# Kernel optimization log

Hardware: AMD Instinct MI355X
Metric: run time of the kernel (lower is better)

Reference implementation:

```python
import jax, jax.numpy as jnp
import numpy as np

B, S, D, H = 2, 2048, 1024, 16
DK = D // H
NEG = -1e9


def setup_inputs() -> dict:
    key = jax.random.key(0)
    ks = jax.random.split(key, 12)
    scale = 1.0 / np.sqrt(D)
    inp = {
        'Q': jax.random.normal(ks[0], (B, S, D), jnp.float32),
        'K': jax.random.normal(ks[1], (B, S, D), jnp.float32),
        'V': jax.random.normal(ks[2], (B, S, D), jnp.float32),
        'mask': jnp.tril(jnp.ones((S, S), jnp.int32))[None, None],  # (1,1,S,S) causal
        # torch nn.Linear layout: W has shape (out, in), y = x @ W.T + b
        'WQ': jax.random.normal(ks[3], (D, D), jnp.float32) * scale,
        'bQ': jnp.zeros((D,), jnp.float32),
        'WK': jax.random.normal(ks[4], (D, D), jnp.float32) * scale,
        'bK': jnp.zeros((D,), jnp.float32),
        'WV': jax.random.normal(ks[5], (D, D), jnp.float32) * scale,
        'bV': jnp.zeros((D,), jnp.float32),
        'WO': jax.random.normal(ks[6], (D, D), jnp.float32) * scale,
        'bO': jnp.zeros((D,), jnp.float32),
    }
    return inp


def reference(Q, K, V, mask, WQ, bQ, WK, bK, WV, bV, WO, bO):
    # projections (torch Linear: x @ W.T + b), then split heads -> (B,H,S,DK)
    def split_heads(x):
        return x.reshape(B, S, H, DK).transpose(0, 2, 1, 3)

    Qh = split_heads(Q @ WQ.T + bQ)
    Kh = split_heads(K @ WK.T + bK)
    Vh = split_heads(V @ WV.T + bV)

    scores = jnp.einsum('bhqd,bhkd->bhqk', Qh, Kh) / jnp.sqrt(jnp.float32(DK))
    scores = jnp.where(mask == 0, NEG, scores)
    attn = jax.nn.softmax(scores, axis=-1)  # (B,H,S,S)
    ctx = jnp.einsum('bhqk,bhkd->bhqd', attn, Vh)
    concat = ctx.transpose(0, 2, 1, 3).reshape(B, S, D)
    out = concat @ WO.T + bO
    return out, attn
```

## Files before the change

kernel.cpp:

```cpp
#include <hip/hip_runtime.h>
#include <hip/hip_bf16.h>
#include <cstdint>
#include <cstddef>

#define S_ 2048
#define D_ 1024
#define H_ 16
#define DK_ 64
#define B_ 2

typedef unsigned short u16;
typedef __attribute__((ext_vector_type(8))) short bf16x8;
typedef __attribute__((ext_vector_type(4))) float f32x4;

__device__ inline u16 f2bf(float f) {
    union { float f; unsigned u; } c; c.f = f;
    unsigned u = c.u;
    unsigned r = (u + 0x7fffu + ((u >> 16) & 1u)) >> 16;
    return (u16)r;
}

__device__ inline uint4 cvt8(const float* __restrict__ src) {
    float4 f0 = *(const float4*)(src);
    float4 f1 = *(const float4*)(src + 4);
    union { u16 h[8]; uint4 v; } u;
    u.h[0] = f2bf(f0.x); u.h[1] = f2bf(f0.y); u.h[2] = f2bf(f0.z); u.h[3] = f2bf(f0.w);
    u.h[4] = f2bf(f1.x); u.h[5] = f2bf(f1.y); u.h[6] = f2bf(f1.z); u.h[7] = f2bf(f1.w);
    return u.v;
}

__global__ void __launch_bounds__(256)
proj_qkv(const float* __restrict__ Qi, const float* __restrict__ Ki,
         const float* __restrict__ Vi,
         const float* __restrict__ WQ, const float* __restrict__ WK,
         const float* __restrict__ WV,
         const float* __restrict__ bQ, const float* __restrict__ bK,
         const float* __restrict__ bV,
         u16* __restrict__ Qo, u16* __restrict__ Ko, u16* __restrict__ Vo)
{
    constexpr int BK  = 32;
    constexpr int BKP = 40;

    __shared__ __align__(16) u16 As[128 * BKP];
    __shared__ __align__(16) u16 Bs[128 * BKP];

    const int tid  = threadIdx.x;
    const int lane = tid & 63;
    const int wave = tid >> 6;
    const int wm = wave >> 1;
    const int wn = wave & 1;
    const int m0 = blockIdx.y * 128;
    const int n0 = blockIdx.x * 128;
    const int z  = blockIdx.z;

    const float* A    = (z == 0) ? Qi : (z == 1) ? Ki : Vi;
    const float* W    = (z == 0) ? WQ : (z == 1) ? WK : WV;
    const float* bias = (z == 0) ? bQ : (z == 1) ? bK : bV;
    u16*         O    = (z == 0) ? Qo : (z == 1) ? Ko : Vo;

    f32x4 acc[4][4];
#pragma unroll
    for (int i = 0; i < 4; ++i)
#pragma unroll
        for (int j = 0; j < 4; ++j)
            acc[i][j] = (f32x4){0.f, 0.f, 0.f, 0.f};

    const int fr = lane & 15;
    const int fk = (lane >> 4) << 3;

    for (int k0 = 0; k0 < D_; k0 += BK) {
#pragma unroll
        for (int i = 0; i < 2; ++i) {
            int linear = i * 256 + tid;
            int row = linear >> 2;
            int kk  = (linear & 3) << 3;
            *(uint4*)&As[row * BKP + kk] = cvt8(&A[(size_t)(m0 + row) * D_ + k0 + kk]);
            *(uint4*)&Bs[row * BKP + kk] = cvt8(&W[(size_t)(n0 + row) * D_ + k0 + kk]);
        }
        __syncthreads();

        bf16x8 af[4], bfv[4];
#pragma unroll
        for (int mt = 0; mt < 4; ++mt)
            af[mt] = *(const bf16x8*)&As[(wm * 64 + mt * 16 + fr) * BKP + fk];
#pragma unroll
        for (int nt = 0; nt < 4; ++nt)
            bfv[nt] = *(const bf16x8*)&Bs[(wn * 64 + nt * 16 + fr) * BKP + fk];
#pragma unroll
        for (int mt = 0; mt < 4; ++mt)
#pragma unroll
            for (int nt = 0; nt < 4; ++nt)
                acc[mt][nt] = __builtin_amdgcn_mfma_f32_16x16x32_bf16(
                    af[mt], bfv[nt], acc[mt][nt], 0, 0, 0);
        __syncthreads();
    }

#pragma unroll
    for (int mt = 0; mt < 4; ++mt)
#pragma unroll
        for (int nt = 0; nt < 4; ++nt)
#pragma unroll
            for (int r = 0; r < 4; ++r) {
                int row = m0 + wm * 64 + mt * 16 + ((lane >> 4) << 2) + r;
                int col = n0 + wn * 64 + nt * 16 + (lane & 15);
                float v = acc[mt][nt][r] + bias[col];
                size_t addr;
                if (z < 2)
                    addr = ((size_t)(row >> 11) << 21) + ((size_t)(col >> 6) << 17)
                         + ((size_t)(row & 2047) << 6) + (size_t)(col & 63);
                else
                    addr = ((size_t)(row >> 11) << 21) + ((size_t)(col >> 6) << 17)
                         + ((size_t)(col & 63) << 11) + (size_t)(row & 2047);
                O[addr] = f2bf(v);
            }
}

template<bool BF32>
__global__ void __launch_bounds__(256)
gemm_bt(const u16* __restrict__ Ab, const void* __restrict__ Bv,
        const float* __restrict__ bias, float* __restrict__ C,
        int M, int N, int K, int lda, int ldb)
{
    constexpr int BK  = 32;
    constexpr int BKP = 40;

    __shared__ __align__(16) u16 As[128 * BKP];
    __shared__ __align__(16) u16 Bs[128 * BKP];

    const int tid  = threadIdx.x;
    const int lane = tid & 63;
    const int wave = tid >> 6;
    const int wm = wave >> 1;
    const int wn = wave & 1;
    const int m0 = blockIdx.y * 128;
    const int n0 = blockIdx.x * 128;

    const float* Bf = (const float*)Bv;
    const u16*   Bb = (const u16*)Bv;

    f32x4 acc[4][4];
#pragma unroll
    for (int i = 0; i < 4; ++i)
#pragma unroll
        for (int j = 0; j < 4; ++j)
            acc[i][j] = (f32x4){0.f, 0.f, 0.f, 0.f};

    const int fr = lane & 15;
    const int fk = (lane >> 4) << 3;

    for (int k0 = 0; k0 < K; k0 += BK) {
#pragma unroll
        for (int i = 0; i < 2; ++i) {
            int linear = i * 256 + tid;
            int row = linear >> 2;
            int kk  = (linear & 3) << 3;
            *(uint4*)&As[row * BKP + kk] =
                *(const uint4*)&Ab[(size_t)(m0 + row) * lda + k0 + kk];
            *(uint4*)&Bs[row * BKP + kk] =
                BF32 ? cvt8(&Bf[(size_t)(n0 + row) * ldb + k0 + kk])
                     : *(const uint4*)&Bb[(size_t)(n0 + row) * ldb + k0 + kk];
        }
        __syncthreads();

        bf16x8 af[4], bfv[4];
#pragma unroll
        for (int mt = 0; mt < 4; ++mt)
            af[mt] = *(const bf16x8*)&As[(wm * 64 + mt * 16 + fr) * BKP + fk];
#pragma unroll
        for (int nt = 0; nt < 4; ++nt)
            bfv[nt] = *(const bf16x8*)&Bs[(wn * 64 + nt * 16 + fr) * BKP + fk];
#pragma unroll
        for (int mt = 0; mt < 4; ++mt)
#pragma unroll
            for (int nt = 0; nt < 4; ++nt)
                acc[mt][nt] = __builtin_amdgcn_mfma_f32_16x16x32_bf16(
                    af[mt], bfv[nt], acc[mt][nt], 0, 0, 0);
        __syncthreads();
    }

#pragma unroll
    for (int mt = 0; mt < 4; ++mt)
#pragma unroll
        for (int nt = 0; nt < 4; ++nt)
#pragma unroll
            for (int r = 0; r < 4; ++r) {
                int row = m0 + wm * 64 + mt * 16 + ((lane >> 4) << 2) + r;
                int col = n0 + wn * 64 + nt * 16 + (lane & 15);
                C[(size_t)row * N + col] = acc[mt][nt][r] + bias[col];
            }
}

__global__ void __launch_bounds__(256, 2)
attn_all(const u16* __restrict__ Qh, const u16* __restrict__ Kh,
         const u16* __restrict__ Vt,
         float* __restrict__ attn, u16* __restrict__ Cc)
{
    __shared__ __align__(16) u16 Qs[128 * 64];
    __shared__ __align__(16) u16 Ks[128 * 64];
    __shared__ __align__(16) u16 Vs[64 * 128];
    __shared__ __align__(16) u16 Ps[128 * 128];
    float* rowsum = (float*)Ps;

    const int tid  = threadIdx.x;
    const int lane = tid & 63;
    const int wave = tid >> 6;
    const int wm = wave >> 1, wn = wave & 1;
    const int bx = blockIdx.x;
    const int qt = (bx & 1) ? (15 - (bx >> 1)) : (bx >> 1);
    const int bh = blockIdx.y;
    const int fr = lane & 15;
    const int fq = lane >> 4;

    const u16* Qbase = Qh + (size_t)bh * S_ * DK_ + (size_t)qt * 128 * DK_;
    const u16* Kbase = Kh + (size_t)bh * S_ * DK_;
    const u16* Vbase = Vt + (size_t)bh * (size_t)DK_ * S_;
    float* out = attn + (size_t)bh * S_ * S_;

#pragma unroll
    for (int i = 0; i < 4; ++i) {
        int linear = i * 256 + tid;
        int row = linear >> 3;
        *(uint4*)((char*)Qs + (row << 7) + ((((linear & 7) << 4)) ^ ((row & 7) << 4)))
            = *(const uint4*)&Qbase[(size_t)linear << 3];
    }
    if (tid < 128) rowsum[tid] = 0.f;

    float rs[4][4];
#pragma unroll
    for (int i = 0; i < 4; ++i)
#pragma unroll
        for (int j = 0; j < 4; ++j) rs[i][j] = 0.f;

    for (int kt = 0; kt <= qt; ++kt) {
        __syncthreads();
#pragma unroll
        for (int i = 0; i < 4; ++i) {
            int linear = i * 256 + tid;
            int row = linear >> 3;
            *(uint4*)((char*)Ks + (row << 7) + ((((linear & 7) << 4)) ^ ((row & 7) << 4)))
                = *(const uint4*)&Kbase[(size_t)kt * 128 * DK_ + ((size_t)linear << 3)];
        }
        __syncthreads();

        f32x4 acc[4][4];
#pragma unroll
        for (int i = 0; i < 4; ++i)
#pragma unroll
            for (int j = 0; j < 4; ++j) acc[i][j] = (f32x4){0.f, 0.f, 0.f, 0.f};

#pragma unroll
        for (int ks = 0; ks < 64; ks += 32) {
            bf16x8 af[4], bfv[4];
#pragma unroll
            for (int mt = 0; mt < 4; ++mt) {
                int row = wm * 64 + mt * 16 + fr;
                af[mt] = *(const bf16x8*)((const char*)Qs + (row << 7)
                          + ((((ks + (fq << 3)) << 1)) ^ ((row & 7) << 4)));
            }
#pragma unroll
            for (int nt = 0; nt < 4; ++nt) {
                int row = wn * 64 + nt * 16 + fr;
                bfv[nt] = *(const bf16x8*)((const char*)Ks + (row << 7)
                          + ((((ks + (fq << 3)) << 1)) ^ ((row & 7) << 4)));
            }
#pragma unroll
            for (int mt = 0; mt < 4; ++mt)
#pragma unroll
                for (int nt = 0; nt < 4; ++nt)
                    acc[mt][nt] = __builtin_amdgcn_mfma_f32_16x16x32_bf16(
                        af[mt], bfv[nt], acc[mt][nt], 0, 0, 0);
        }

        const bool diag = (kt == qt);
#pragma unroll
        for (int mt = 0; mt < 4; ++mt)
#pragma unroll
            for (int nt = 0; nt < 4; ++nt)
#pragma unroll
                for (int r = 0; r < 4; ++r) {
                    int row = wm * 64 + mt * 16 + (fq << 2) + r;
                    int col = wn * 64 + nt * 16 + fr;
                    if (!diag || col <= row)
                        rs[mt][r] += __expf(acc[mt][nt][r] * 0.125f);
                }
    }

#pragma unroll
    for (int mt = 0; mt < 4; ++mt)
#pragma unroll
        for (int r = 0; r < 4; ++r) {
            float v = rs[mt][r];
            v += __shfl_xor(v, 1, 64);
            v += __shfl_xor(v, 2, 64);
            v += __shfl_xor(v, 4, 64);
            v += __shfl_xor(v, 8, 64);
            rs[mt][r] = v;
        }
    __syncthreads();
    if (fr == 0) {
#pragma unroll
        for (int mt = 0; mt < 4; ++mt)
#pragma unroll
            for (int r = 0; r < 4; ++r)
                atomicAdd(&rowsum[wm * 64 + mt * 16 + (fq << 2) + r], rs[mt][r]);
    }
    __syncthreads();

    float rcp[4][4];
#pragma unroll
    for (int mt = 0; mt < 4; ++mt)
#pragma unroll
        for (int r = 0; r < 4; ++r)
            rcp[mt][r] = 1.0f / rowsum[wm * 64 + mt * 16 + (fq << 2) + r];

    f32x4 cacc[4][2];
#pragma unroll
    for (int i = 0; i < 4; ++i)
#pragma unroll
        for (int j = 0; j < 2; ++j) cacc[i][j] = (f32x4){0.f, 0.f, 0.f, 0.f};

    for (int kt = 0; kt <= qt; ++kt) {
        __syncthreads();
#pragma unroll
        for (int i = 0; i < 4; ++i) {
            int linear = i * 256 + tid;
            int row = linear >> 3;
            *(uint4*)((char*)Ks + (row << 7) + ((((linear & 7) << 4)) ^ ((row & 7) << 4)))
                = *(const uint4*)&Kbase[(size_t)kt * 128 * DK_ + ((size_t)linear << 3)];
        }
#pragma unroll
        for (int i = 0; i < 4; ++i) {
            int linear = i * 256 + tid;
            int row = linear >> 4;
            int cb  = (linear & 15) << 4;
            *(uint4*)((char*)Vs + (row << 8) + (cb ^ ((row & 7) << 4)))
                = *(const uint4*)&Vbase[(size_t)row * S_ + kt * 128 + ((linear & 15) << 3)];
        }
        __syncthreads();

        f32x4 acc[4][4];
#pragma unroll
        for (int i = 0; i < 4; ++i)
#pragma unroll
            for (int j = 0; j < 4; ++j) acc[i][j] = (f32x4){0.f, 0.f, 0.f, 0.f};

#pragma unroll
        for (int ks = 0; ks < 64; ks += 32) {
            bf16x8 af[4], bfv[4];
#pragma unroll
            for (int mt = 0; mt < 4; ++mt) {
                int row = wm * 64 + mt * 16 + fr;
                af[mt] = *(const bf16x8*)((const char*)Qs + (row << 7)
                          + ((((ks + (fq << 3)) << 1)) ^ ((row & 7) << 4)));
            }
#pragma unroll
            for (int nt = 0; nt < 4; ++nt) {
                int row = wn * 64 + nt * 16 + fr;
                bfv[nt] = *(const bf16x8*)((const char*)Ks + (row << 7)
                          + ((((ks + (fq << 3)) << 1)) ^ ((row & 7) << 4)));
            }
#pragma unroll
            for (int mt = 0; mt < 4; ++mt)
#pragma unroll
                for (int nt = 0; nt < 4; ++nt)
                    acc[mt][nt] = __builtin_amdgcn_mfma_f32_16x16x32_bf16(
                        af[mt], bfv[nt], acc[mt][nt], 0, 0, 0);
        }

        const bool diag = (kt == qt);
#pragma unroll
        for (int mt = 0; mt < 4; ++mt)
#pragma unroll
            for (int nt = 0; nt < 4; ++nt)
#pragma unroll
                for (int r = 0; r < 4; ++r) {
                    int row = wm * 64 + mt * 16 + (fq << 2) + r;
                    int col = wn * 64 + nt * 16 + fr;
                    float p = 0.f;
                    if (!diag || col <= row)
                        p = __expf(acc[mt][nt][r] * 0.125f) * rcp[mt][r];
                    out[(size_t)(qt * 128 + row) * S_ + kt * 128 + col] = p;
                    *(u16*)((char*)Ps + (row << 8) + (((col << 1)) ^ ((row & 7) << 4)))
                        = f2bf(p);
                }
        __syncthreads();

#pragma unroll
        for (int ks4 = 0; ks4 < 4; ++ks4) {
            bf16x8 pf[4], vf[2];
            int kb = (ks4 * 32 + (fq << 3)) << 1;
#pragma unroll
            for (int mt = 0; mt < 4; ++mt) {
                int row = wm * 64 + mt * 16 + fr;
                pf[mt] = *(const bf16x8*)((const char*)Ps + (row << 8)
                          + (kb ^ ((row & 7) << 4)));
            }
#pragma unroll
            for (int nt = 0; nt < 2; ++nt) {
                int row = wn * 32 + nt * 16 + fr;
                vf[nt] = *(const bf16x8*)((const char*)Vs + (row << 8)
                          + (kb ^ ((row & 7) << 4)));
            }
#pragma unroll
            for (int mt = 0; mt < 4; ++mt)
#pragma unroll
                for (int nt = 0; nt < 2; ++nt)
                    cacc[mt][nt] = __builtin_amdgcn_mfma_f32_16x16x32_bf16(
                        pf[mt], vf[nt], cacc[mt][nt], 0, 0, 0);
        }
    }

#pragma unroll
    for (int mt = 0; mt < 4; ++mt)
#pragma unroll
        for (int nt = 0; nt < 2; ++nt)
#pragma unroll
            for (int r = 0; r < 4; ++r) {
                int row = wm * 64 + mt * 16 + (fq << 2) + r;
                int col = wn * 32 + nt * 16 + fr;
                size_t addr = (size_t)(bh >> 4) * S_ * D_ + (size_t)(bh & 15) * DK_
                            + (size_t)(qt * 128 + row) * D_ + col;
                Cc[addr] = f2bf(cacc[mt][nt][r]);
            }

    float4 z4 = {0.f, 0.f, 0.f, 0.f};
    for (int kt2 = qt + 1; kt2 < S_ / 128; ++kt2) {
#pragma unroll
        for (int i = 0; i < 16; ++i) {
            int linear = i * 256 + tid;
            int row = linear >> 5;
            int c   = (linear & 31) << 2;
            *(float4*)&out[(size_t)(qt * 128 + row) * S_ + kt2 * 128 + c] = z4;
        }
    }
}

extern "C" void kernel_launch(void* const* d_in, const int* in_sizes, int n_in,
                              void* d_out, int out_size, void* d_ws, size_t ws_size,
                              hipStream_t stream)
{
    const float* Q  = (const float*)d_in[0];
    const float* K  = (const float*)d_in[1];
    const float* V  = (const float*)d_in[2];
    const float* WQ = (const float*)d_in[4];
    const float* bQ = (const float*)d_in[5];
    const float* WK = (const float*)d_in[6];
    const float* bK = (const float*)d_in[7];
    const float* WV = (const float*)d_in[8];
    const float* bV = (const float*)d_in[9];
    const float* WO = (const float*)d_in[10];
    const float* bO = (const float*)d_in[11];

    float* outF  = (float*)d_out;
    float* attnF = outF + (size_t)B_ * S_ * D_;

    u16* Qh = (u16*)d_ws;
    u16* Kh = Qh + (size_t)B_ * S_ * D_;
    u16* Vt = Kh + (size_t)B_ * S_ * D_;
    u16* Cc = Vt + (size_t)B_ * S_ * D_;

    dim3 blk(256, 1, 1);
    const int M = B_ * S_;

    proj_qkv<<<dim3(D_ / 128, M / 128, 3), blk, 0, stream>>>(
        Q, K, V, WQ, WK, WV, bQ, bK, bV, Qh, Kh, Vt);

    attn_all<<<dim3(S_ / 128, B_ * H_, 1), blk, 0, stream>>>(
        Qh, Kh, Vt, attnF, Cc);

    gemm_bt<true><<<dim3(D_ / 128, M / 128, 1), blk, 0, stream>>>(
        Cc, WO, bO, outF, M, D_, D_, D_, D_);
}
```

Measured before the change: 806.9 us.

## Pre-convert inputs to bf16, use direct global-to-LDS loads and vectorized attention stores

Adds a separate kernel that converts Q, K, V and all weights to bf16 once, so the projection and output GEMMs load bf16 through global_load_lds with swizzled LDS tiles and BK=64. The attention kernel swaps the MFMA operand order so each lane owns contiguous key columns, which lets the attention-probability writes be float4 and the P tile be packed with v_cvt_pk_bf16_f32. The GEMM epilogues now also store vectorized. The aim is to cut conversion work inside the GEMM inner loops and reduce scattered scalar stores of the large attention matrix, at the cost of an extra kernel launch and more workspace traffic.

```diff
diff --git a/kernel.cpp b/kernel.cpp
--- a/kernel.cpp
+++ b/kernel.cpp
@@ -29,165 +29,209 @@
     return u.v;
 }
 
+__device__ inline unsigned pkbf(float a, float b) {
+    unsigned r;
+    asm("v_cvt_pk_bf16_f32 %0, %1, %2" : "=v"(r) : "v"(a), "v"(b));
+    return r;
+}
+
+typedef __attribute__((address_space(3))) void lds_void;
+typedef __attribute__((address_space(1))) const void glob_void;
+__device__ __forceinline__ void glds16(const u16* g, u16* l, int lane) {
+#if __has_builtin(__builtin_amdgcn_global_load_lds)
+    (void)lane;
+    __builtin_amdgcn_global_load_lds((glob_void*)g, (lds_void*)l, 16, 0, 0);
+#else
+    ((uint4*)l)[lane] = *(const uint4*)g;
+#endif
+}
+
+__device__ __forceinline__ bf16x8 rd64(const u16* arr, int row, int k) {
+    return *(const bf16x8*)((const char*)arr + (row << 7)
+             + ((k << 1) ^ ((row & 7) << 4)));
+}
+__device__ __forceinline__ bf16x8 rd128(const u16* arr, int row, int k) {
+    return *(const bf16x8*)((const char*)arr + (row << 8)
+             + ((k << 1) ^ ((row & 7) << 4)));
+}
+
 __global__ void __launch_bounds__(256)
-proj_qkv(const float* __restrict__ Qi, const float* __restrict__ Ki,
-         const float* __restrict__ Vi,
-         const float* __restrict__ WQ, const float* __restrict__ WK,
-         const float* __restrict__ WV,
+cvt_all(const float* __restrict__ Q, const float* __restrict__ K,
+        const float* __restrict__ V,
+        const float* __restrict__ WQ, const float* __restrict__ WK,
+        const float* __restrict__ WV, const float* __restrict__ WO,
+        u16* __restrict__ Qb, u16* __restrict__ Kb, u16* __restrict__ Vb,
+        u16* __restrict__ Wb)
+{
+    const size_t QN = 524288;
+    const size_t WN = 131072;
+    size_t u = (size_t)blockIdx.x * 256 + threadIdx.x;
+    const size_t total = 3 * QN + 4 * WN;
+    const size_t stride = (size_t)gridDim.x * 256;
+    for (; u < total; u += stride) {
+        const float* s; u16* d; size_t off;
+        if (u < 3 * QN) {
+            size_t seg = u / QN;
+            off = (u - seg * QN) << 3;
+            s = (seg == 0) ? Q : (seg == 1) ? K : V;
+            d = (seg == 0) ? Qb : (seg == 1) ? Kb : Vb;
+        } else {
+            size_t w = u - 3 * QN;
+            size_t seg = w / WN;
+            off = (w - seg * WN) << 3;
+            s = (seg == 0) ? WQ : (seg == 1) ? WK : (seg == 2) ? WV : WO;
+            d = Wb + seg * 1048576;
+        }
+        *(uint4*)&d[off] = cvt8(s + off);
+    }
+}
+
+__device__ __forceinline__ void gemm_core(
+    const u16* __restrict__ A, const u16* __restrict__ Bm,
+    int m0, int n0, int tid, u16* As, u16* Bs, f32x4 (&acc)[4][4])
+{
+    const int lane = tid & 63;
+    const int wave = tid >> 6;
+    const int wm = wave >> 1, wn = wave & 1;
+    const int fr = lane & 15, fq = lane >> 4;
+
+    for (int k0 = 0; k0 < 1024; k0 += 64) {
+        __syncthreads();
+#pragma unroll
+        for (int it = 0; it < 4; ++it) {
+            int linear = it * 256 + tid;
+            int row = linear >> 3, c = linear & 7;
+            glds16(&A[(size_t)(m0 + row) * 1024 + k0 + ((c ^ (row & 7)) << 3)],
+                   &As[(size_t)(it * 256 + (tid & ~63)) << 3], lane);
+        }
+#pragma unroll
+        for (int it = 0; it < 4; ++it) {
+            int linear = it * 256 + tid;
+            int row = linear >> 3, c = linear & 7;
+            glds16(&Bm[(size_t)(n0 + row) * 1024 + k0 + ((c ^ (row & 7)) << 3)],
+                   &Bs[(size_t)(it * 256 + (tid & ~63)) << 3], lane);
+        }
+        __syncthreads();
+#pragma unroll
+        for (int ks = 0; ks < 64; ks += 32) {
+            bf16x8 af[4], bfv[4];
+#pragma unroll
+            for (int mt = 0; mt < 4; ++mt)
+                af[mt] = rd64(As, wm * 64 + mt * 16 + fr, ks + (fq << 3));
+#pragma unroll
+            for (int nt = 0; nt < 4; ++nt)
+                bfv[nt] = rd64(Bs, wn * 64 + nt * 16 + fr, ks + (fq << 3));
+#pragma unroll
+            for (int mt = 0; mt < 4; ++mt)
+#pragma unroll
+                for (int nt = 0; nt < 4; ++nt)
+                    acc[mt][nt] = __builtin_amdgcn_mfma_f32_16x16x32_bf16(
+                        bfv[nt], af[mt], acc[mt][nt], 0, 0, 0);
+        }
+    }
+}
+
+__global__ void __launch_bounds__(256)
+proj_qkv(const u16* __restrict__ Qb, const u16* __restrict__ Kb,
+         const u16* __restrict__ Vb, const u16* __restrict__ Wb,
          const float* __restrict__ bQ, const float* __restrict__ bK,
          const float* __restrict__ bV,
-         u16* __restrict__ Qo, u16* __restrict__ Ko, u16* __restrict__ Vo)
+         u16* __restrict__ Qh, u16* __restrict__ Kh, u16* __restrict__ Vt)
 {
-    constexpr int BK  = 32;
-    constexpr int BKP = 40;
-
-    __shared__ __align__(16) u16 As[128 * BKP];
-    __shared__ __align__(16) u16 Bs[128 * BKP];
+    __shared__ __align__(16) u16 As[128 * 64];
+    __shared__ __align__(16) u16 Bs[128 * 64];
 
     const int tid  = threadIdx.x;
     const int lane = tid & 63;
     const int wave = tid >> 6;
-    const int wm = wave >> 1;
-    const int wn = wave & 1;
+    const int wm = wave >> 1, wn = wave & 1;
+    const int fr = lane & 15, fq = lane >> 4;
     const int m0 = blockIdx.y * 128;
     const int n0 = blockIdx.x * 128;
     const int z  = blockIdx.z;
 
-    const float* A    = (z == 0) ? Qi : (z == 1) ? Ki : Vi;
-    const float* W    = (z == 0) ? WQ : (z == 1) ? WK : WV;
+    const u16* A = (z == 0) ? Qb : (z == 1) ? Kb : Vb;
+    const u16* W = Wb + (size_t)z * 1048576;
     const float* bias = (z == 0) ? bQ : (z == 1) ? bK : bV;
-    u16*         O    = (z == 0) ? Qo : (z == 1) ? Ko : Vo;
+    u16* O = (z == 0) ? Qh : (z == 1) ? Kh : Vt;
 
     f32x4 acc[4][4];
 #pragma unroll
     for (int i = 0; i < 4; ++i)
 #pragma unroll
-        for (int j = 0; j < 4; ++j)
-            acc[i][j] = (f32x4){0.f, 0.f, 0.f, 0.f};
-
-    const int fr = lane & 15;
-    const int fk = (lane >> 4) << 3;
-
-    for (int k0 = 0; k0 < D_; k0 += BK) {
-#pragma unroll
-        for (int i = 0; i < 2; ++i) {
-            int linear = i * 256 + tid;
-            int row = linear >> 2;
-            int kk  = (linear & 3) << 3;
-            *(uint4*)&As[row * BKP + kk] = cvt8(&A[(size_t)(m0 + row) * D_ + k0 + kk]);
-            *(uint4*)&Bs[row * BKP + kk] = cvt8(&W[(size_t)(n0 + row) * D_ + k0 + kk]);
-        }
-        __syncthreads();
-
-        bf16x8 af[4], bfv[4];
-#pragma unroll
-        for (int mt = 0; mt < 4; ++mt)
-            af[mt] = *(const bf16x8*)&As[(wm * 64 + mt * 16 + fr) * BKP + fk];
-#pragma unroll
-        for (int nt = 0; nt < 4; ++nt)
-            bfv[nt] = *(const bf16x8*)&Bs[(wn * 64 + nt * 16 + fr) * BKP + fk];
-#pragma unroll
-        for (int mt = 0; mt < 4; ++mt)
-#pragma unroll
-            for (int nt = 0; nt < 4; ++nt)
-                acc[mt][nt] = __builtin_amdgcn_mfma_f32_16x16x32_bf16(
-                    af[mt], bfv[nt], acc[mt][nt], 0, 0, 0);
-        __syncthreads();
-    }
-
-#pragma unroll
-    for (int mt = 0; mt < 4; ++mt)
-#pragma unroll
-        for (int nt = 0; nt < 4; ++nt)
-#pragma unroll
-            for (int r = 0; r < 4; ++r) {
-                int row = m0 + wm * 64 + mt * 16 + ((lane >> 4) << 2) + r;
-                int col = n0 + wn * 64 + nt * 16 + (lane & 15);
-                float v = acc[mt][nt][r] + bias[col];
-                size_t addr;
-                if (z < 2)
-                    addr = ((size_t)(row >> 11) << 21) + ((size_t)(col >> 6) << 17)
-                         + ((size_t)(row & 2047) << 6) + (size_t)(col & 63);
-                else
-                    addr = ((size_t)(row >> 11) << 21) + ((size_t)(col >> 6) << 17)
-                         + ((size_t)(col & 63) << 11) + (size_t)(row & 2047);
-                O[addr] = f2bf(v);
+        for (int j = 0; j < 4; ++j) acc[i][j] = (f32x4){0.f, 0.f, 0.f, 0.f};
+
+    gemm_core(A, W, m0, n0, tid, As, Bs, acc);
+
+#pragma unroll
+    for (int mt = 0; mt < 4; ++mt) {
+#pragma unroll
+        for (int nt = 0; nt < 4; ++nt) {
+            int row  = m0 + wm * 64 + mt * 16 + fr;
+            int colb = n0 + wn * 64 + nt * 16 + (fq << 2);
+            float4 b4 = *(const float4*)&bias[colb];
+            u16 h[4];
+            h[0] = f2bf(acc[mt][nt][0] + b4.x);
+            h[1] = f2bf(acc[mt][nt][1] + b4.y);
+            h[2] = f2bf(acc[mt][nt][2] + b4.z);
+            h[3] = f2bf(acc[mt][nt][3] + b4.w);
+            if (z < 2) {
+                size_t addr = ((size_t)(row >> 11) << 21) + ((size_t)(colb >> 6) << 17)
+                            + ((size_t)(row & 2047) << 6) + (size_t)(colb & 63);
+                uint2 p; p.x = (unsigned)h[0] | ((unsigned)h[1] << 16);
+                         p.y = (unsigned)h[2] | ((unsigned)h[3] << 16);
+                *(uint2*)&O[addr] = p;
+            } else {
+#pragma unroll
+                for (int r = 0; r < 4; ++r) {
+                    int col = colb + r;
+                    size_t addr = ((size_t)(row >> 11) << 21) + ((size_t)(col >> 6) << 17)
+                                + ((size_t)(col & 63) << 11) + (size_t)(row & 2047);
+                    O[addr] = h[r];
+                }
             }
-}
-
-template<bool BF32>
+        }
+    }
+}
+
 __global__ void __launch_bounds__(256)
-gemm_bt(const u16* __restrict__ Ab, const void* __restrict__ Bv,
-        const float* __restrict__ bias, float* __restrict__ C,
-        int M, int N, int K, int lda, int ldb)
+out_gemm(const u16* __restrict__ Cc, const u16* __restrict__ WOb,
+         const float* __restrict__ bO, float* __restrict__ C)
 {
-    constexpr int BK  = 32;
-    constexpr int BKP = 40;
-
-    __shared__ __align__(16) u16 As[128 * BKP];
-    __shared__ __align__(16) u16 Bs[128 * BKP];
+    __shared__ __align__(16) u16 As[128 * 64];
+    __shared__ __align__(16) u16 Bs[128 * 64];
 
     const int tid  = threadIdx.x;
     const int lane = tid & 63;
     const int wave = tid >> 6;
-    const int wm = wave >> 1;
-    const int wn = wave & 1;
+    const int wm = wave >> 1, wn = wave & 1;
+    const int fr = lane & 15, fq = lane >> 4;
     const int m0 = blockIdx.y * 128;
     const int n0 = blockIdx.x * 128;
 
-    const float* Bf = (const float*)Bv;
-    const u16*   Bb = (const u16*)Bv;
-
     f32x4 acc[4][4];
 #pragma unroll
     for (int i = 0; i < 4; ++i)
 #pragma unroll
-        for (int j = 0; j < 4; ++j)
-            acc[i][j] = (f32x4){0.f, 0.f, 0.f, 0.f};
-
-    const int fr = lane & 15;
-    const int fk = (lane >> 4) << 3;
-
-    for (int k0 = 0; k0 < K; k0 += BK) {
-#pragma unroll
-        for (int i = 0; i < 2; ++i) {
-            int linear = i * 256 + tid;
-            int row = linear >> 2;
-            int kk  = (linear & 3) << 3;
-            *(uint4*)&As[row * BKP + kk] =
-                *(const uint4*)&Ab[(size_t)(m0 + row) * lda + k0 + kk];
-            *(uint4*)&Bs[row * BKP + kk] =
-                BF32 ? cvt8(&Bf[(size_t)(n0 + row) * ldb + k0 + kk])
-                     : *(const uint4*)&Bb[(size_t)(n0 + row) * ldb + k0 + kk];
-        }
-        __syncthreads();
-
-        bf16x8 af[4], bfv[4];
-#pragma unroll
-        for (int mt = 0; mt < 4; ++mt)
-            af[mt] = *(const bf16x8*)&As[(wm * 64 + mt * 16 + fr) * BKP + fk];
-#pragma unroll
-        for (int nt = 0; nt < 4; ++nt)
-            bfv[nt] = *(const bf16x8*)&Bs[(wn * 64 + nt * 16 + fr) * BKP + fk];
-#pragma unroll
-        for (int mt = 0; mt < 4; ++mt)
-#pragma unroll
-            for (int nt = 0; nt < 4; ++nt)
-                acc[mt][nt] = __builtin_amdgcn_mfma_f32_16x16x32_bf16(
-                    af[mt], bfv[nt], acc[mt][nt], 0, 0, 0);
-        __syncthreads();
-    }
-
-#pragma unroll
-    for (int mt = 0; mt < 4; ++mt)
-#pragma unroll
-        for (int nt = 0; nt < 4; ++nt)
-#pragma unroll
-            for (int r = 0; r < 4; ++r) {
-                int row = m0 + wm * 64 + mt * 16 + ((lane >> 4) << 2) + r;
-                int col = n0 + wn * 64 + nt * 16 + (lane & 15);
-                C[(size_t)row * N + col] = acc[mt][nt][r] + bias[col];
-            }
+        for (int j = 0; j < 4; ++j) acc[i][j] = (f32x4){0.f, 0.f, 0.f, 0.f};
+
+    gemm_core(Cc, WOb, m0, n0, tid, As, Bs, acc);
+
+#pragma unroll
+    for (int mt = 0; mt < 4; ++mt) {
+#pragma unroll
+        for (int nt = 0; nt < 4; ++nt) {
+            int row  = m0 + wm * 64 + mt * 16 + fr;
+            int colb = n0 + wn * 64 + nt * 16 + (fq << 2);
+            float4 b4 = *(const float4*)&bO[colb];
+            float4 v;
+            v.x = acc[mt][nt][0] + b4.x;
+            v.y = acc[mt][nt][1] + b4.y;
+            v.z = acc[mt][nt][2] + b4.z;
+            v.w = acc[mt][nt][3] + b4.w;
+            *(float4*)&C[(size_t)row * D_ + colb] = v;
+        }
+    }
 }
 
 __global__ void __launch_bounds__(256, 2)
@@ -199,7 +243,7 @@
     __shared__ __align__(16) u16 Ks[128 * 64];
     __shared__ __align__(16) u16 Vs[64 * 128];
     __shared__ __align__(16) u16 Ps[128 * 128];
-    float* rowsum = (float*)Ps;
+    float* rowsum = (float*)Vs;
 
     const int tid  = threadIdx.x;
     const int lane = tid & 63;
@@ -208,8 +252,7 @@
     const int bx = blockIdx.x;
     const int qt = (bx & 1) ? (15 - (bx >> 1)) : (bx >> 1);
     const int bh = blockIdx.y;
-    const int fr = lane & 15;
-    const int fq = lane >> 4;
+    const int fr = lane & 15, fq = lane >> 4;
 
     const u16* Qbase = Qh + (size_t)bh * S_ * DK_ + (size_t)qt * 128 * DK_;
     const u16* Kbase = Kh + (size_t)bh * S_ * DK_;
@@ -217,28 +260,105 @@
     float* out = attn + (size_t)bh * S_ * S_;
 
 #pragma unroll
-    for (int i = 0; i < 4; ++i) {
-        int linear = i * 256 + tid;
-        int row = linear >> 3;
-        *(uint4*)((char*)Qs + (row << 7) + ((((linear & 7) << 4)) ^ ((row & 7) << 4)))
-            = *(const uint4*)&Qbase[(size_t)linear << 3];
+    for (int it = 0; it < 4; ++it) {
+        int linear = it * 256 + tid;
+        int row = linear >> 3, c = linear & 7;
+        glds16(&Qbase[(size_t)row * 64 + ((c ^ (row & 7)) << 3)],
+               &Qs[(size_t)(it * 256 + (tid & ~63)) << 3], lane);
     }
     if (tid < 128) rowsum[tid] = 0.f;
 
-    float rs[4][4];
+    float rs[4] = {0.f, 0.f, 0.f, 0.f};
+
+    for (int kt = 0; kt <= qt; ++kt) {
+        __syncthreads();
+#pragma unroll
+        for (int it = 0; it < 4; ++it) {
+            int linear = it * 256 + tid;
+            int row = linear >> 3, c = linear & 7;
+            glds16(&Kbase[(size_t)kt * 128 * 64 + (size_t)row * 64 + ((c ^ (row & 7)) << 3)],
+                   &Ks[(size_t)(it * 256 + (tid & ~63)) << 3], lane);
+        }
+        __syncthreads();
+
+        f32x4 acc[4][4];
+#pragma unroll
+        for (int i = 0; i < 4; ++i)
+#pragma unroll
+            for (int j = 0; j < 4; ++j) acc[i][j] = (f32x4){0.f, 0.f, 0.f, 0.f};
+
+#pragma unroll
+        for (int ks = 0; ks < 64; ks += 32) {
+            bf16x8 kf4[4], qf4[4];
+#pragma unroll
+            for (int i = 0; i < 4; ++i)
+                kf4[i] = rd64(Ks, wm * 64 + i * 16 + fr, ks + (fq << 3));
+#pragma unroll
+            for (int j = 0; j < 4; ++j)
+                qf4[j] = rd64(Qs, wn * 64 + j * 16 + fr, ks + (fq << 3));
+#pragma unroll
+            for (int i = 0; i < 4; ++i)
+#pragma unroll
+                for (int j = 0; j < 4; ++j)
+                    acc[i][j] = __builtin_amdgcn_mfma_f32_16x16x32_bf16(
+                        kf4[i], qf4[j], acc[i][j], 0, 0, 0);
+        }
+
+        const bool diag = (kt == qt);
+#pragma unroll
+        for (int kf = 0; kf < 4; ++kf) {
+#pragma unroll
+            for (int qf = 0; qf < 4; ++qf) {
+                const int kb = wm * 64 + kf * 16, qb = wn * 64 + qf * 16;
+                if (!diag || kb < qb) {
+#pragma unroll
+                    for (int r = 0; r < 4; ++r)
+                        rs[qf] += __expf(acc[kf][qf][r] * 0.125f);
+                } else if (diag && kb == qb) {
+#pragma unroll
+                    for (int r = 0; r < 4; ++r)
+                        if ((fq << 2) + r <= fr)
+                            rs[qf] += __expf(acc[kf][qf][r] * 0.125f);
+                }
+            }
+        }
+    }
+
+#pragma unroll
+    for (int qf = 0; qf < 4; ++qf) {
+        float v = rs[qf];
+        v += __shfl_xor(v, 16, 64);
+        v += __shfl_xor(v, 32, 64);
+        if (lane < 16) atomicAdd(&rowsum[wn * 64 + qf * 16 + lane], v);
+    }
+    __syncthreads();
+
+    float rcp_l[4];
+#pragma unroll
+    for (int qf = 0; qf < 4; ++qf)
+        rcp_l[qf] = 1.0f / rowsum[wn * 64 + qf * 16 + fr];
+
+    f32x4 cacc[4][2];
 #pragma unroll
     for (int i = 0; i < 4; ++i)
 #pragma unroll
-        for (int j = 0; j < 4; ++j) rs[i][j] = 0.f;
+        for (int j = 0; j < 2; ++j) cacc[i][j] = (f32x4){0.f, 0.f, 0.f, 0.f};
 
     for (int kt = 0; kt <= qt; ++kt) {
         __syncthreads();
 #pragma unroll
-        for (int i = 0; i < 4; ++i) {
-            int linear = i * 256 + tid;
-            int row = linear >> 3;
-            *(uint4*)((char*)Ks + (row << 7) + ((((linear & 7) << 4)) ^ ((row & 7) << 4)))
-                = *(const uint4*)&Kbase[(size_t)kt * 128 * DK_ + ((size_t)linear << 3)];
+        for (int it = 0; it < 4; ++it) {
+            int linear = it * 256 + tid;
+            int row = linear >> 3, c = linear & 7;
+            glds16(&Kbase[(size_t)kt * 128 * 64 + (size_t)row * 64 + ((c ^ (row & 7)) << 3)],
+                   &Ks[(size_t)(it * 256 + (tid & ~63)) << 3], lane);
+        }
+#pragma unroll
+        for (int it = 0; it < 4; ++it) {
+            int linear = it * 256 + tid;
+            int row = linear >> 4, c = linear & 15;
+            glds16(&Vbase[(size_t)row * S_ + kt * 128 + ((c ^ (row & 7)) << 3)],
+                   &Vs[(size_t)(it * 256 + (tid & ~63)) << 3], lane);
         }
         __syncthreads();
 
@@ -250,157 +370,63 @@
 
 #pragma unroll
         for (int ks = 0; ks < 64; ks += 32) {
-            bf16x8 af[4], bfv[4];
-#pragma unroll
-            for (int mt = 0; mt < 4; ++mt) {
-                int row = wm * 64 + mt * 16 + fr;
-                af[mt] = *(const bf16x8*)((const char*)Qs + (row << 7)
-                          + ((((ks + (fq << 3)) << 1)) ^ ((row & 7) << 4)));
+            bf16x8 kf4[4], qf4[4];
+#pragma unroll
+            for (int i = 0; i < 4; ++i)
+                kf4[i] = rd64(Ks, wm * 64 + i * 16 + fr, ks + (fq << 3));
+#pragma unroll
+            for (int j = 0; j < 4; ++j)
+                qf4[j] = rd64(Qs, wn * 64 + j * 16 + fr, ks + (fq << 3));
+#pragma unroll
+            for (int i = 0; i < 4; ++i)
+#pragma unroll
+                for (int j = 0; j < 4; ++j)
+                    acc[i][j] = __builtin_amdgcn_mfma_f32_16x16x32_bf16(
+                        kf4[i], qf4[j], acc[i][j], 0, 0, 0);
+        }
+
+        const bool diag = (kt == qt);
+#pragma unroll
+        for (int kf = 0; kf < 4; ++kf) {
+#pragma unroll
+            for (int qf = 0; qf < 4; ++qf) {
+                const int kb = wm * 64 + kf * 16, qb = wn * 64 + qf * 16;
+                const int qrow = qb + fr;
+                float4 p4;
+                if (!diag || kb < qb) {
+                    p4.x = __expf(acc[kf][qf][0] * 0.125f) * rcp_l[qf];
+                    p4.y = __expf(acc[kf][qf][1] * 0.125f) * rcp_l[qf];
+                    p4.z = __expf(acc[kf][qf][2] * 0.125f) * rcp_l[qf];
+                    p4.w = __expf(acc[kf][qf][3] * 0.125f) * rcp_l[qf];
+                } else if (kb > qb) {
+                    p4 = (float4){0.f, 0.f, 0.f, 0.f};
+                } else {
+#pragma unroll
+                    for (int r = 0; r < 4; ++r) {
+                        float e = __expf(acc[kf][qf][r] * 0.125f) * rcp_l[qf];
+                        ((float*)&p4)[r] = ((fq << 2) + r <= fr) ? e : 0.f;
+                    }
+                }
+                *(float4*)&out[(size_t)(qt * 128 + qrow) * S_ + kt * 128 + kb + (fq << 2)] = p4;
+                uint2 pk;
+                pk.x = pkbf(p4.x, p4.y);
+                pk.y = pkbf(p4.z, p4.w);
+                *(uint2*)((char*)Ps + (qrow << 8)
+                          + (((kb + (fq << 2)) << 1) ^ ((qrow & 7) << 4))) = pk;
             }
-#pragma unroll
-            for (int nt = 0; nt < 4; ++nt) {
-                int row = wn * 64 + nt * 16 + fr;
-                bfv[nt] = *(const bf16x8*)((const char*)Ks + (row << 7)
-                          + ((((ks + (fq << 3)) << 1)) ^ ((row & 7) << 4)));
-            }
-#pragma unroll
-            for (int mt = 0; mt < 4; ++mt)
-#pragma unroll
-                for (int nt = 0; nt < 4; ++nt)
-                    acc[mt][nt] = __builtin_amdgcn_mfma_f32_16x16x32_bf16(
-                        af[mt], bfv[nt], acc[mt][nt], 0, 0, 0);
-        }
-
-        const bool diag = (kt == qt);
-#pragma unroll
-        for (int mt = 0; mt < 4; ++mt)
-#pragma unroll
-            for (int nt = 0; nt < 4; ++nt)
-#pragma unroll
-                for (int r = 0; r < 4; ++r) {
-                    int row = wm * 64 + mt * 16 + (fq << 2) + r;
-                    int col = wn * 64 + nt * 16 + fr;
-                    if (!diag || col <= row)
-                        rs[mt][r] += __expf(acc[mt][nt][r] * 0.125f);
-                }
-    }
-
-#pragma unroll
-    for (int mt = 0; mt < 4; ++mt)
-#pragma unroll
-        for (int r = 0; r < 4; ++r) {
-            float v = rs[mt][r];
-            v += __shfl_xor(v, 1, 64);
-            v += __shfl_xor(v, 2, 64);
-            v += __shfl_xor(v, 4, 64);
-            v += __shfl_xor(v, 8, 64);
-            rs[mt][r] = v;
-        }
-    __syncthreads();
-    if (fr == 0) {
-#pragma unroll
-        for (int mt = 0; mt < 4; ++mt)
-#pragma unroll
-            for (int r = 0; r < 4; ++r)
-                atomicAdd(&rowsum[wm * 64 + mt * 16 + (fq << 2) + r], rs[mt][r]);
-    }
-    __syncthreads();
-
-    float rcp[4][4];
-#pragma unroll
-    for (int mt = 0; mt < 4; ++mt)
-#pragma unroll
-        for (int r = 0; r < 4; ++r)
-            rcp[mt][r] = 1.0f / rowsum[wm * 64 + mt * 16 + (fq << 2) + r];
-
-    f32x4 cacc[4][2];
-#pragma unroll
-    for (int i = 0; i < 4; ++i)
-#pragma unroll
-        for (int j = 0; j < 2; ++j) cacc[i][j] = (f32x4){0.f, 0.f, 0.f, 0.f};
-
-    for (int kt = 0; kt <= qt; ++kt) {
-        __syncthreads();
-#pragma unroll
-        for (int i = 0; i < 4; ++i) {
-            int linear = i * 256 + tid;
-            int row = linear >> 3;
-            *(uint4*)((char*)Ks + (row << 7) + ((((linear & 7) << 4)) ^ ((row & 7) << 4)))
-                = *(const uint4*)&Kbase[(size_t)kt * 128 * DK_ + ((size_t)linear << 3)];
-        }
-#pragma unroll
-        for (int i = 0; i < 4; ++i) {
-            int linear = i * 256 + tid;
-            int row = linear >> 4;
-            int cb  = (linear & 15) << 4;
-            *(uint4*)((char*)Vs + (row << 8) + (cb ^ ((row & 7) << 4)))
-                = *(const uint4*)&Vbase[(size_t)row * S_ + kt * 128 + ((linear & 15) << 3)];
-        }
-        __syncthreads();
-
-        f32x4 acc[4][4];
-#pragma unroll
-        for (int i = 0; i < 4; ++i)
-#pragma unroll
-            for (int j = 0; j < 4; ++j) acc[i][j] = (f32x4){0.f, 0.f, 0.f, 0.f};
-
-#pragma unroll
-        for (int ks = 0; ks < 64; ks += 32) {
-            bf16x8 af[4], bfv[4];
-#pragma unroll
-            for (int mt = 0; mt < 4; ++mt) {
-                int row = wm * 64 + mt * 16 + fr;
-                af[mt] = *(const bf16x8*)((const char*)Qs + (row << 7)
-                          + ((((ks + (fq << 3)) << 1)) ^ ((row & 7) << 4)));
-            }
-#pragma unroll
-            for (int nt = 0; nt < 4; ++nt) {
-                int row = wn * 64 + nt * 16 + fr;
-                bfv[nt] = *(const bf16x8*)((const char*)Ks + (row << 7)
-                          + ((((ks + (fq << 3)) << 1)) ^ ((row & 7) << 4)));
-            }
-#pragma unroll
-            for (int mt = 0; mt < 4; ++mt)
-#pragma unroll
-                for (int nt = 0; nt < 4; ++nt)
-                    acc[mt][nt] = __builtin_amdgcn_mfma_f32_16x16x32_bf16(
-                        af[mt], bfv[nt], acc[mt][nt], 0, 0, 0);
-        }
-
-        const bool diag = (kt == qt);
-#pragma unroll
-        for (int mt = 0; mt < 4; ++mt)
-#pragma unroll
-            for (int nt = 0; nt < 4; ++nt)
-#pragma unroll
-                for (int r = 0; r < 4; ++r) {
-                    int row = wm * 64 + mt * 16 + (fq << 2) + r;
-                    int col = wn * 64 + nt * 16 + fr;
-                    float p = 0.f;
-                    if (!diag || col <= row)
-                        p = __expf(acc[mt][nt][r] * 0.125f) * rcp[mt][r];
-                    out[(size_t)(qt * 128 + row) * S_ + kt * 128 + col] = p;
-                    *(u16*)((char*)Ps + (row << 8) + (((col << 1)) ^ ((row & 7) << 4)))
-                        = f2bf(p);
-                }
+        }
         __syncthreads();
 
 #pragma unroll
         for (int ks4 = 0; ks4 < 4; ++ks4) {
             bf16x8 pf[4], vf[2];
-            int kb = (ks4 * 32 + (fq << 3)) << 1;
-#pragma unroll
-            for (int mt = 0; mt < 4; ++mt) {
-                int row = wm * 64 + mt * 16 + fr;
-                pf[mt] = *(const bf16x8*)((const char*)Ps + (row << 8)
-                          + (kb ^ ((row & 7) << 4)));
-            }
-#pragma unroll
-            for (int nt = 0; nt < 2; ++nt) {
-                int row = wn * 32 + nt * 16 + fr;
-                vf[nt] = *(const bf16x8*)((const char*)Vs + (row << 8)
-                          + (kb ^ ((row & 7) << 4)));
-            }
+            const int kk = ks4 * 32 + (fq << 3);
+#pragma unroll
+            for (int mt = 0; mt < 4; ++mt)
+                pf[mt] = rd128(Ps, wm * 64 + mt * 16 + fr, kk);
+#pragma unroll
+            for (int nt = 0; nt < 2; ++nt)
+                vf[nt] = rd128(Vs, wn * 32 + nt * 16 + fr, kk);
 #pragma unroll
             for (int mt = 0; mt < 4; ++mt)
 #pragma unroll
@@ -454,20 +480,27 @@
     float* outF  = (float*)d_out;
     float* attnF = outF + (size_t)B_ * S_ * D_;
 
+    const size_t SZ = (size_t)B_ * S_ * D_;
     u16* Qh = (u16*)d_ws;
-    u16* Kh = Qh + (size_t)B_ * S_ * D_;
-    u16* Vt = Kh + (size_t)B_ * S_ * D_;
-    u16* Cc = Vt + (size_t)B_ * S_ * D_;
+    u16* Kh = Qh + SZ;
+    u16* Vt = Kh + SZ;
+    u16* Cc = Vt + SZ;
+    u16* Qb = Cc + SZ;
+    u16* Kb = Qb + SZ;
+    u16* Vb = Kb + SZ;
+    u16* Wb = Vb + SZ;
 
     dim3 blk(256, 1, 1);
-    const int M = B_ * S_;
-
-    proj_qkv<<<dim3(D_ / 128, M / 128, 3), blk, 0, stream>>>(
-        Q, K, V, WQ, WK, WV, bQ, bK, bV, Qh, Kh, Vt);
+
+    cvt_all<<<dim3(1024, 1, 1), blk, 0, stream>>>(
+        Q, K, V, WQ, WK, WV, WO, Qb, Kb, Vb, Wb);
+
+    proj_qkv<<<dim3(8, 32, 3), blk, 0, stream>>>(
+        Qb, Kb, Vb, Wb, bQ, bK, bV, Qh, Kh, Vt);
 
     attn_all<<<dim3(S_ / 128, B_ * H_, 1), blk, 0, stream>>>(
         Qh, Kh, Vt, attnF, Cc);
 
-    gemm_bt<true><<<dim3(D_ / 128, M / 128, 1), blk, 0, stream>>>(
-        Cc, WO, bO, outF, M, D_, D_, D_, D_);
-}
+    out_gemm<<<dim3(8, 32, 1), blk, 0, stream>>>(
+        Cc, Wb + 3 * 1048576, bO, outF);
+}
```

Result: faster. 771.0 us (-4.4%).
